# Kernel tuning notes

Hardware: AMD Instinct MI355X
Metric: run time of the kernel (lower is better)

## Reference

```python
import jax, jax.numpy as jnp
import numpy as np


def setup_inputs() -> dict:
    key = jax.random.key(0)
    k1, k2, k3 = jax.random.split(key, 3)
    RAW_NODES = 40962          # ico-6 sphere
    NUM_NODES = RAW_NODES * 4 - 6   # 163842, ico-7 sphere
    FEAT = 256
    x = jax.random.normal(k1, (RAW_NODES, FEAT), dtype=jnp.float32)
    max_index = jax.random.randint(k2, (RAW_NODES, FEAT), 0, 7, dtype=jnp.int64)
    neigh_orders = jax.random.randint(k3, (RAW_NODES * 7,), 0, NUM_NODES, dtype=jnp.int64)
    return {"x": x, "max_index": max_index, "neigh_orders": neigh_orders, "num_nodes": NUM_NODES}


def reference(x, max_index, neigh_orders, num_nodes):
    raw_nodes, feat_num = x.shape
    # column_ref[i, f] = i*7 + max_index[i, f]  (vectorized form of the python loop)
    column_ref = (jnp.arange(raw_nodes, dtype=max_index.dtype)[:, None] * 7 + max_index).reshape(-1)
    column_index = neigh_orders[column_ref]  # gather from neighborhood lookup table
    # row_index exactly as in the original: floor(linspace(0, feat_num, raw_nodes*feat_num)), last clamped
    row_index = np.floor(np.linspace(0.0, float(feat_num), num=raw_nodes * feat_num)).astype(np.int64)
    row_index[-1] = row_index[-1] - 1
    row_index = jnp.asarray(row_index)
    y = jnp.zeros((num_nodes, feat_num), dtype=x.dtype)
    # scatter: y[column_index, row_index] = x.view(-1)
    y = y.at[column_index, row_index].set(x.reshape(-1))
    return y
```

## Files before the change

### kernel.cpp

```cpp
#include <hip/hip_runtime.h>
#include <stdint.h>


#define FEAT 256
#define LOG2FEAT 8
#define BLOCK 256
#define BUILD_WGS 256
#define ZERO_WGS 1024
#define EPN 16

extern "C" __global__ __launch_bounds__(BLOCK)
void build_zero_kernel(const int*   __restrict__ mi,
                       const int*   __restrict__ neigh,
                       float*       __restrict__ out,
                       int2*        __restrict__ entries,
                       int total,
                       int out_elems)
{
    const int tid = threadIdx.x;

    if (blockIdx.x >= BUILD_WGS) {
        const int zid = blockIdx.x - BUILD_WGS;
        float4* out4 = (float4*)out;
        const int total4 = out_elems >> 2;
        const float4 z = make_float4(0.f, 0.f, 0.f, 0.f);
        for (int idx = zid * BLOCK + tid; idx < total4; idx += ZERO_WGS * BLOCK)
            out4[idx] = z;
        return;
    }

    const int lane      = tid & 63;
    const int wv        = (blockIdx.x * BLOCK + tid) >> 6;
    const int nwaves    = BUILD_WGS * (BLOCK / 64);
    const int raw_nodes = total >> LOG2FEAT;
    const unsigned tm1  = (unsigned)(total - 1);

    int p0 = 0, p1 = 0, p2 = 0, p3 = 0;
    if (wv < raw_nodes) {
        const int* mrow = mi + (wv << LOG2FEAT);
        p0 = mrow[lane]; p1 = mrow[64 + lane];
        p2 = mrow[128 + lane]; p3 = mrow[192 + lane];
    }

    for (int i = wv; i < raw_nodes; i += nwaves) {
        const int m0 = p0, m1 = p1, m2 = p2, m3 = p3;
        const int i_n = i + nwaves;
        if (i_n < raw_nodes) {
            const int* mrow = mi + (i_n << LOG2FEAT);
            p0 = mrow[lane]; p1 = mrow[64 + lane];
            p2 = mrow[128 + lane]; p3 = mrow[192 + lane];
        }

        const int kbase = i << LOG2FEAT;
        unsigned long long b[4][7];
        #pragma unroll
        for (int m = 0; m < 7; ++m) {
            b[0][m] = __ballot(m0 == m);
            b[1][m] = __ballot(m1 == m);
            b[2][m] = __ballot(m2 == m);
            b[3][m] = __ballot(m3 == m);
        }

        unsigned r_first = (((unsigned)kbase) << 8) / tm1;
        unsigned r_last  = (((unsigned)(kbase + FEAT - 1)) << 8) / tm1;
        if (r_last > 255u) r_last = 255u;
        const bool straddle = (r_last != r_first);
        unsigned fb = FEAT;
        if (straddle) fb = ((r_last * tm1 + 255u) >> 8) - (unsigned)kbase;

        unsigned long long g[4];
        #pragma unroll
        for (int j = 0; j < 4; ++j)
            g[j] = (fb >= (unsigned)(j + 1) * 64) ? ~0ull
                 : (fb <= (unsigned)j * 64)       ? 0ull
                 : ((1ull << (fb - (unsigned)j * 64)) - 1ull);

        int  m  = -1;
        bool hi = false;
        if (lane < 7)                                { m = lane;     hi = false; }
        else if (straddle && lane >= 8 && lane < 15) { m = lane - 8; hi = true;  }

        int2 ent = make_int2(0, 0);
        if (m >= 0) {
            int bestf = -1;
            #pragma unroll
            for (int j = 3; j >= 0; --j) {
                if (bestf < 0) {
                    unsigned long long s =
                        (m == 0) ? b[j][0] : (m == 1) ? b[j][1] :
                        (m == 2) ? b[j][2] : (m == 3) ? b[j][3] :
                        (m == 4) ? b[j][4] : (m == 5) ? b[j][5] : b[j][6];
                    unsigned long long t = s & (hi ? ~g[j] : g[j]);
                    if (t) bestf = j * 64 + 63 - __clzll(t);
                }
            }
            if (bestf >= 0) {
                const int k   = kbase + bestf;
                const int col = neigh[i * 7 + m];
                const int r   = hi ? (int)r_last : (int)r_first;
                ent = make_int2((col << LOG2FEAT) | r, k + 1);
            }
        }
        if (lane < EPN)
            entries[(size_t)i * EPN + lane] = ent;
    }
}

extern "C" __global__ __launch_bounds__(256)
void tag_kernel(int* __restrict__ out_i,
                const int2* __restrict__ entries,
                int n_entries)
{
    for (int idx = blockIdx.x * 256 + threadIdx.x; idx < n_entries;
         idx += gridDim.x * 256) {
        const int2 e = entries[idx];
        if (e.y > 0) atomicMax(out_i + e.x, e.y);
    }
}

extern "C" __global__ __launch_bounds__(256)
void value_kernel(int* __restrict__ out_i,
                  const float* __restrict__ x,
                  const int2* __restrict__ entries,
                  int n_entries)
{
    for (int idx = blockIdx.x * 256 + threadIdx.x; idx < n_entries;
         idx += gridDim.x * 256) {
        const int2 e = entries[idx];
        if (e.y > 0 && out_i[e.x] == e.y)
            out_i[e.x] = __float_as_int(x[e.y - 1]);
    }
}

extern "C" void kernel_launch(void* const* d_in, const int* in_sizes, int n_in,
                              void* d_out, int out_size, void* d_ws, size_t ws_size,
                              hipStream_t stream) {
    const float* x     = (const float*)d_in[0];
    const int*   mi    = (const int*)d_in[1];
    const int*   neigh = (const int*)d_in[2];
    float*       out   = (float*)d_out;

    const int total     = in_sizes[0];
    const int out_elems = out_size;
    const int raw_nodes = total >> LOG2FEAT;
    const int n_entries = raw_nodes * EPN;

    int2* entries = (int2*)d_ws;

    build_zero_kernel<<<dim3(BUILD_WGS + ZERO_WGS), dim3(BLOCK), 0, stream>>>(
        mi, neigh, out, entries, total, out_elems);
    tag_kernel<<<dim3(1024), dim3(256), 0, stream>>>(
        (int*)out, entries, n_entries);
    value_kernel<<<dim3(1024), dim3(256), 0, stream>>>(
        (int*)out, x, entries, n_entries);
}
```

Before: 281.3 us.

## Fuse build, tag and value kernels into one cooperative kernel with grid syncs

```diff
diff --git a/kernel.cpp b/kernel.cpp
--- a/kernel.cpp
+++ b/kernel.cpp
@@ -1,134 +1,138 @@
 #include <hip/hip_runtime.h>
+#include <hip/hip_cooperative_groups.h>
 #include <stdint.h>
+
+namespace cg = cooperative_groups;
 
 
 #define FEAT 256
 #define LOG2FEAT 8
 #define BLOCK 256
 #define BUILD_WGS 256
-#define ZERO_WGS 1024
-#define EPN 16
+#define TOTAL_WGS 1280
+#define EPN 8
 
-extern "C" __global__ __launch_bounds__(BLOCK)
-void build_zero_kernel(const int*   __restrict__ mi,
-                       const int*   __restrict__ neigh,
-                       float*       __restrict__ out,
-                       int2*        __restrict__ entries,
-                       int total,
-                       int out_elems)
+__global__ void __launch_bounds__(BLOCK)
+upsample_all_kernel(const float* __restrict__ x,
+                    const int*   __restrict__ mi,
+                    const int*   __restrict__ neigh,
+                    float*       __restrict__ out,
+                    int2*        __restrict__ entries,
+                    int total,
+                    int out_elems)
 {
-    const int tid = threadIdx.x;
+    const int tid       = threadIdx.x;
+    const int raw_nodes = total >> LOG2FEAT;
+    const int n_main    = raw_nodes * EPN;
+    const int n_entries = n_main + 255 * EPN;
+    int* out_i = (int*)out;
 
     if (blockIdx.x >= BUILD_WGS) {
         const int zid = blockIdx.x - BUILD_WGS;
         float4* out4 = (float4*)out;
         const int total4 = out_elems >> 2;
         const float4 z = make_float4(0.f, 0.f, 0.f, 0.f);
-        for (int idx = zid * BLOCK + tid; idx < total4; idx += ZERO_WGS * BLOCK)
+        for (int idx = zid * BLOCK + tid; idx < total4;
+             idx += (TOTAL_WGS - BUILD_WGS) * BLOCK)
             out4[idx] = z;
-        return;
-    }
+    } else {
+        const int lane     = tid & 63;
+        const int wv       = (blockIdx.x * BLOCK + tid) >> 6;
+        const int nwaves   = BUILD_WGS * (BLOCK / 64);
+        const unsigned tm1 = (unsigned)(total - 1);
 
-    const int lane      = tid & 63;
-    const int wv        = (blockIdx.x * BLOCK + tid) >> 6;
-    const int nwaves    = BUILD_WGS * (BLOCK / 64);
-    const int raw_nodes = total >> LOG2FEAT;
-    const unsigned tm1  = (unsigned)(total - 1);
-
-    int p0 = 0, p1 = 0, p2 = 0, p3 = 0;
-    if (wv < raw_nodes) {
-        const int* mrow = mi + (wv << LOG2FEAT);
-        p0 = mrow[lane]; p1 = mrow[64 + lane];
-        p2 = mrow[128 + lane]; p3 = mrow[192 + lane];
-    }
-
-    for (int i = wv; i < raw_nodes; i += nwaves) {
-        const int m0 = p0, m1 = p1, m2 = p2, m3 = p3;
-        const int i_n = i + nwaves;
-        if (i_n < raw_nodes) {
-            const int* mrow = mi + (i_n << LOG2FEAT);
+        int p0 = 0, p1 = 0, p2 = 0, p3 = 0;
+        if (wv < raw_nodes) {
+            const int* mrow = mi + (wv << LOG2FEAT);
             p0 = mrow[lane]; p1 = mrow[64 + lane];
             p2 = mrow[128 + lane]; p3 = mrow[192 + lane];
         }
 
-        const int kbase = i << LOG2FEAT;
-        unsigned long long b[4][7];
-        #pragma unroll
-        for (int m = 0; m < 7; ++m) {
-            b[0][m] = __ballot(m0 == m);
-            b[1][m] = __ballot(m1 == m);
-            b[2][m] = __ballot(m2 == m);
-            b[3][m] = __ballot(m3 == m);
-        }
+        for (int i = wv; i < raw_nodes; i += nwaves) {
+            const int m0 = p0, m1 = p1, m2 = p2, m3 = p3;
+            const int i_n = i + nwaves;
+            if (i_n < raw_nodes) {
+                const int* mrow = mi + (i_n << LOG2FEAT);
+                p0 = mrow[lane]; p1 = mrow[64 + lane];
+                p2 = mrow[128 + lane]; p3 = mrow[192 + lane];
+            }
 
-        unsigned r_first = (((unsigned)kbase) << 8) / tm1;
-        unsigned r_last  = (((unsigned)(kbase + FEAT - 1)) << 8) / tm1;
-        if (r_last > 255u) r_last = 255u;
-        const bool straddle = (r_last != r_first);
-        unsigned fb = FEAT;
-        if (straddle) fb = ((r_last * tm1 + 255u) >> 8) - (unsigned)kbase;
+            const int kbase = i << LOG2FEAT;
+            unsigned long long b[4][7];
+            #pragma unroll
+            for (int m = 0; m < 7; ++m) {
+                b[0][m] = __ballot(m0 == m);
+                b[1][m] = __ballot(m1 == m);
+                b[2][m] = __ballot(m2 == m);
+                b[3][m] = __ballot(m3 == m);
+            }
 
-        unsigned long long g[4];
-        #pragma unroll
-        for (int j = 0; j < 4; ++j)
-            g[j] = (fb >= (unsigned)(j + 1) * 64) ? ~0ull
-                 : (fb <= (unsigned)j * 64)       ? 0ull
-                 : ((1ull << (fb - (unsigned)j * 64)) - 1ull);
+            unsigned r_first = (((unsigned)kbase) << 8) / tm1;
+            unsigned r_last  = (((unsigned)(kbase + FEAT - 1)) << 8) / tm1;
+            if (r_last > 255u) r_last = 255u;
+            const bool straddle = (r_last != r_first);
+            unsigned fb = FEAT;
+            if (straddle) fb = ((r_last * tm1 + 255u) >> 8) - (unsigned)kbase;
 
-        int  m  = -1;
-        bool hi = false;
-        if (lane < 7)                                { m = lane;     hi = false; }
-        else if (straddle && lane >= 8 && lane < 15) { m = lane - 8; hi = true;  }
+            unsigned long long g[4];
+            #pragma unroll
+            for (int j = 0; j < 4; ++j)
+                g[j] = (fb >= (unsigned)(j + 1) * 64) ? ~0ull
+                     : (fb <= (unsigned)j * 64)       ? 0ull
+                     : ((1ull << (fb - (unsigned)j * 64)) - 1ull);
 
-        int2 ent = make_int2(0, 0);
-        if (m >= 0) {
-            int bestf = -1;
-            #pragma unroll
-            for (int j = 3; j >= 0; --j) {
-                if (bestf < 0) {
-                    unsigned long long s =
-                        (m == 0) ? b[j][0] : (m == 1) ? b[j][1] :
-                        (m == 2) ? b[j][2] : (m == 3) ? b[j][3] :
-                        (m == 4) ? b[j][4] : (m == 5) ? b[j][5] : b[j][6];
-                    unsigned long long t = s & (hi ? ~g[j] : g[j]);
-                    if (t) bestf = j * 64 + 63 - __clzll(t);
+            int  m  = -1;
+            bool hi = false;
+            if (lane < 7)                                { m = lane;     hi = false; }
+            else if (straddle && lane >= 8 && lane < 15) { m = lane - 8; hi = true;  }
+
+            int2 ent = make_int2(0, 0);
+            if (m >= 0) {
+                int bestf = -1;
+                #pragma unroll
+                for (int j = 3; j >= 0; --j) {
+                    if (bestf < 0) {
+                        unsigned long long s =
+                            (m == 0) ? b[j][0] : (m == 1) ? b[j][1] :
+                            (m == 2) ? b[j][2] : (m == 3) ? b[j][3] :
+                            (m == 4) ? b[j][4] : (m == 5) ? b[j][5] : b[j][6];
+                        unsigned long long t = s & (hi ? ~g[j] : g[j]);
+                        if (t) bestf = j * 64 + 63 - __clzll(t);
+                    }
+                }
+                if (bestf >= 0) {
+                    const int k   = kbase + bestf;
+                    const int col = neigh[i * 7 + m];
+                    const int r   = hi ? (int)r_last : (int)r_first;
+                    ent = make_int2((col << LOG2FEAT) | r, k + 1);
                 }
             }
-            if (bestf >= 0) {
-                const int k   = kbase + bestf;
-                const int col = neigh[i * 7 + m];
-                const int r   = hi ? (int)r_last : (int)r_first;
-                ent = make_int2((col << LOG2FEAT) | r, k + 1);
-            }
+            if (lane < EPN)
+                entries[(size_t)i * EPN + lane] = ent;
+            if (straddle && lane >= 8 && lane < 8 + EPN)
+                entries[(size_t)n_main + ((size_t)r_last - 1) * EPN + (lane - 8)] = ent;
         }
-        if (lane < EPN)
-            entries[(size_t)i * EPN + lane] = ent;
     }
-}
 
-extern "C" __global__ __launch_bounds__(256)
-void tag_kernel(int* __restrict__ out_i,
-                const int2* __restrict__ entries,
-                int n_entries)
-{
-    for (int idx = blockIdx.x * 256 + threadIdx.x; idx < n_entries;
-         idx += gridDim.x * 256) {
-        const int2 e = entries[idx];
-        if (e.y > 0) atomicMax(out_i + e.x, e.y);
+    cg::this_grid().sync();
+
+    {
+        const int gtid = blockIdx.x * BLOCK + tid;
+        for (int idx = gtid; idx < n_entries; idx += TOTAL_WGS * BLOCK) {
+            const int2 e = entries[idx];
+            if (e.y > 0) atomicMax(out_i + e.x, e.y);
+        }
     }
-}
 
-extern "C" __global__ __launch_bounds__(256)
-void value_kernel(int* __restrict__ out_i,
-                  const float* __restrict__ x,
-                  const int2* __restrict__ entries,
-                  int n_entries)
-{
-    for (int idx = blockIdx.x * 256 + threadIdx.x; idx < n_entries;
-         idx += gridDim.x * 256) {
-        const int2 e = entries[idx];
-        if (e.y > 0 && out_i[e.x] == e.y)
-            out_i[e.x] = __float_as_int(x[e.y - 1]);
+    cg::this_grid().sync();
+
+    {
+        const int gtid = blockIdx.x * BLOCK + tid;
+        for (int idx = gtid; idx < n_entries; idx += TOTAL_WGS * BLOCK) {
+            const int2 e = entries[idx];
+            if (e.y > 0 && out_i[e.x] == e.y)
+                out_i[e.x] = __float_as_int(x[e.y - 1]);
+        }
     }
 }
 
@@ -140,17 +144,12 @@
     const int*   neigh = (const int*)d_in[2];
     float*       out   = (float*)d_out;
 
-    const int total     = in_sizes[0];
-    const int out_elems = out_size;
-    const int raw_nodes = total >> LOG2FEAT;
-    const int n_entries = raw_nodes * EPN;
-
+    int total     = in_sizes[0];
+    int out_elems = out_size;
     int2* entries = (int2*)d_ws;
 
-    build_zero_kernel<<<dim3(BUILD_WGS + ZERO_WGS), dim3(BLOCK), 0, stream>>>(
-        mi, neigh, out, entries, total, out_elems);
-    tag_kernel<<<dim3(1024), dim3(256), 0, stream>>>(
-        (int*)out, entries, n_entries);
-    value_kernel<<<dim3(1024), dim3(256), 0, stream>>>(
-        (int*)out, x, entries, n_entries);
+    void* args[] = { (void*)&x, (void*)&mi, (void*)&neigh, (void*)&out,
+                     (void*)&entries, (void*)&total, (void*)&out_elems };
+    hipLaunchCooperativeKernel((const void*)upsample_all_kernel,
+                               dim3(TOTAL_WGS), dim3(BLOCK), args, 0, stream);
 }
```

Measured after the change: 582.8 us. 2.07x slower.
